# Performance work log

Measured on AMD Instinct MI355X. Metric: run time of the kernel, lower is better.

The kernel has to match this reference:

```python
import jax, jax.numpy as jnp
import numpy as np

N_NODES = 50000
NEG_SLOPE = 0.2


def gat_conv(x, edge_index, W, a_src, a_dst, b):
    """PyG GATConv, heads=1: linear -> per-edge attention -> segment softmax -> scatter-add."""
    n = x.shape[0]
    h = x @ W                                   # [N, out]
    # add self-loops (PyG default add_self_loops=True)
    loop = jnp.arange(n, dtype=edge_index.dtype)
    src = jnp.concatenate([edge_index[0], loop])  # message sources j
    dst = jnp.concatenate([edge_index[1], loop])  # aggregation targets i
    alpha_s = h @ a_src                          # [N]
    alpha_d = h @ a_dst                          # [N]
    e = jax.nn.leaky_relu(alpha_s[src] + alpha_d[dst], NEG_SLOPE)  # [E+N]
    # numerically stable segment softmax over edges grouped by dst
    m = jax.ops.segment_max(e, dst, num_segments=n)
    ex = jnp.exp(e - m[dst])
    denom = jax.ops.segment_sum(ex, dst, num_segments=n)
    alpha = ex / denom[dst]                      # [E+N]
    out = jax.ops.segment_sum(h[src] * alpha[:, None], dst, num_segments=n)
    return out + b


def setup_inputs() -> dict:
    key = jax.random.key(0)
    ks = jax.random.split(key, 12)
    F_IN, H1, H2 = 128, 64, 32
    E, ED = 800000, 800000
    x = jax.random.normal(ks[0], (N_NODES, F_IN), dtype=jnp.float32)
    edge_index = jax.random.randint(ks[1], (2, E), 0, N_NODES, dtype=jnp.int64)
    pos_edge_index = jax.random.randint(ks[2], (2, ED), 0, N_NODES, dtype=jnp.int64)
    neg_edge_index = jax.random.randint(ks[3], (2, ED), 0, N_NODES, dtype=jnp.int64)
    g = lambda k, shape, fan: (jax.random.normal(k, shape, dtype=jnp.float32) * (1.0 / np.sqrt(fan))).astype(jnp.float32)
    W1 = g(ks[4], (F_IN, H1), F_IN)
    a_src1 = g(ks[5], (H1,), H1)
    a_dst1 = g(ks[6], (H1,), H1)
    b1 = jnp.zeros((H1,), dtype=jnp.float32)
    W2 = g(ks[7], (H1, H2), H1)
    a_src2 = g(ks[8], (H2,), H2)
    a_dst2 = g(ks[9], (H2,), H2)
    b2 = jnp.zeros((H2,), dtype=jnp.float32)
    return {"x": x, "edge_index": edge_index, "pos_edge_index": pos_edge_index,
            "neg_edge_index": neg_edge_index, "W1": W1, "a_src1": a_src1,
            "a_dst1": a_dst1, "b1": b1, "W2": W2, "a_src2": a_src2,
            "a_dst2": a_dst2, "b2": b2}


def reference(x, edge_index, pos_edge_index, neg_edge_index,
              W1, a_src1, a_dst1, b1, W2, a_src2, a_dst2, b2):
    # encode (dropout omitted: eval-mode)
    h = gat_conv(x, edge_index, W1, a_src1, a_dst1, b1)
    h = jax.nn.relu(h)
    z = gat_conv(h, edge_index, W2, a_src2, a_dst2, b2)
    # decode: per-edge dot products on concatenated pos/neg edges
    ei = jnp.concatenate([pos_edge_index, neg_edge_index], axis=-1)
    logits = jnp.sum(z[ei[0]] * z[ei[1]], axis=-1)
    return logits
```

## Files before the change

kernel.cpp:

```cpp
#include <hip/hip_runtime.h>

#define NEG_SLOPE 0.2f

constexpr int N_NODES = 50000;
constexpr int TPB = 256;
constexpr int BSH = 7;
constexpr int NB = (N_NODES + 127) >> BSH;
constexpr int SCAT_CHUNK = 8192;

__device__ __forceinline__ unsigned short f2b(float f) {
  unsigned u = __float_as_uint(f);
  return (unsigned short)((u + 0x7FFFu + ((u >> 16) & 1u)) >> 16);
}
__device__ __forceinline__ float b2f(unsigned short b) {
  return __uint_as_float(((unsigned)b) << 16);
}
__device__ __forceinline__ float blo(unsigned u) {
  return __uint_as_float(u << 16);
}
__device__ __forceinline__ float bhi(unsigned u) {
  return __uint_as_float(u & 0xFFFF0000u);
}
__device__ __forceinline__ unsigned pack2(float a, float b) {
  return (unsigned)f2b(a) | ((unsigned)f2b(b) << 16);
}

__device__ __forceinline__ void tw_elem(const float* __restrict__ W,
                                        float4* __restrict__ Wt, int OUTD,
                                        int i) {
  int k4 = i / OUTD, c = i % OUTD;
  Wt[i] = make_float4(W[(4 * k4 + 0) * OUTD + c], W[(4 * k4 + 1) * OUTD + c],
                      W[(4 * k4 + 2) * OUTD + c], W[(4 * k4 + 3) * OUTD + c]);
}

__global__ void prep_kernel(const float* __restrict__ W1,
                            float4* __restrict__ Wt1,
                            const float* __restrict__ W2,
                            float4* __restrict__ Wt2,
                            int* __restrict__ pairCnt) {
  int i = blockIdx.x * blockDim.x + threadIdx.x;
  if (i < 2048) {
    tw_elem(W1, Wt1, 64, i);
  } else if (i < 2048 + 512) {
    tw_elem(W2, Wt2, 32, i - 2048);
  } else if (i < 2048 + 512 + NB) {
    pairCnt[i - 2560] = 0;
  }
}

template <int K, int OUTD>
__global__ __launch_bounds__(TPB) void gemm_alpha_hist(
    const float* __restrict__ X, const float4* __restrict__ Wt,
    const float* __restrict__ avec_src, const float* __restrict__ avec_dst,
    unsigned short* __restrict__ Hout, float* __restrict__ as_out,
    float* __restrict__ ad_out, int n, const int* __restrict__ edst, int E,
    int* __restrict__ pairCnt, int gemmBlocks) {
  constexpr int BK = 16;
  constexpr int NT = K / BK;
  constexpr int CT = OUTD / 2;
  constexpr int RG = 64 / CT;
  constexpr int RPT = 16 / RG;
  constexpr int WPB = TPB / 64;
  __shared__ float xs[WPB][2][16][BK + 4];
  __shared__ int hh[NB];

  if (blockIdx.x >= gemmBlocks) {
    const int vb = blockIdx.x - gemmBlocks;
    for (int i = threadIdx.x; i < NB; i += TPB) hh[i] = 0;
    __syncthreads();
    for (int i = vb * TPB + threadIdx.x; i < E; i += 256 * TPB)
      atomicAdd(&hh[edst[i] >> BSH], 1);
    __syncthreads();
    for (int i = threadIdx.x; i < NB; i += TPB)
      if (hh[i]) atomicAdd(&pairCnt[i], hh[i]);
    return;
  }

  const int t = threadIdx.x;
  const int wid = t >> 6;
  const int lane = t & 63;
  const int waveRow0 = blockIdx.x * (WPB * 16) + wid * 16;

  const int srow = lane >> 2;
  const int skq = lane & 3;
  const float* srcRow = X + (size_t)min(waveRow0 + srow, n - 1) * K + skq * 4;

  const int cc = lane % CT;
  const int c0 = 2 * cc;
  const int rg = lane / CT;
  const int r0 = rg * RPT;

  const float a_s0 = avec_src[c0], a_s1 = avec_src[c0 + 1];
  const float a_d0 = avec_dst[c0], a_d1 = avec_dst[c0 + 1];

  float4 g = *(const float4*)srcRow;
  *(float4*)&xs[wid][0][srow][skq * 4] = g;

  float acc[RPT][2];
#pragma unroll
  for (int i = 0; i < RPT; ++i) acc[i][0] = acc[i][1] = 0.f;

  for (int tile = 0;;) {
    if (tile + 1 < NT)
      g = *(const float4*)(srcRow + (size_t)(tile + 1) * BK);
    const int buf = tile & 1;
#pragma unroll
    for (int kq = 0; kq < BK / 4; ++kq) {
      const int kqg = tile * (BK / 4) + kq;
      const float4 w0 = Wt[(size_t)kqg * OUTD + c0];
      const float4 w1 = Wt[(size_t)kqg * OUTD + c0 + 1];
#pragma unroll
      for (int i = 0; i < RPT; ++i) {
        const float4 xv = *(const float4*)&xs[wid][buf][r0 + i][kq * 4];
        acc[i][0] = fmaf(xv.x, w0.x, acc[i][0]);
        acc[i][1] = fmaf(xv.x, w1.x, acc[i][1]);
        acc[i][0] = fmaf(xv.y, w0.y, acc[i][0]);
        acc[i][1] = fmaf(xv.y, w1.y, acc[i][1]);
        acc[i][0] = fmaf(xv.z, w0.z, acc[i][0]);
        acc[i][1] = fmaf(xv.z, w1.z, acc[i][1]);
        acc[i][0] = fmaf(xv.w, w0.w, acc[i][0]);
        acc[i][1] = fmaf(xv.w, w1.w, acc[i][1]);
      }
    }
    if (++tile == NT) break;
    *(float4*)&xs[wid][tile & 1][srow][skq * 4] = g;
  }

#pragma unroll
  for (int i = 0; i < RPT; ++i) {
    const int r = waveRow0 + r0 + i;
    if (r < n) {
      ushort2 hb;
      hb.x = f2b(acc[i][0]);
      hb.y = f2b(acc[i][1]);
      ((ushort2*)Hout)[(size_t)r * CT + cc] = hb;
      float vs = acc[i][0] * a_s0 + acc[i][1] * a_s1;
      float vd = acc[i][0] * a_d0 + acc[i][1] * a_d1;
#pragma unroll
      for (int m = CT / 2; m >= 1; m >>= 1) {
        vs += __shfl_xor(vs, m);
        vd += __shfl_xor(vd, m);
      }
      if (cc == 0) {
        as_out[r] = vs;
        ad_out[r] = vd;
      }
    }
  }
}

__global__ void bucket_scan(const int* __restrict__ pairCnt,
                            int* __restrict__ pairOff,
                            int* __restrict__ pairCursor,
                            int* __restrict__ csrOff, int N) {
  __shared__ int a[512], b[512];
  const int t = threadIdx.x;
  const int pc = (t < NB) ? pairCnt[t] : 0;
  const int nodes = (t < NB) ? min(128, N - (t << BSH)) : 0;
  a[t] = pc;
  b[t] = pc + nodes;
  __syncthreads();
  for (int off = 1; off < 512; off <<= 1) {
    int av = (t >= off) ? a[t - off] : 0;
    int bv = (t >= off) ? b[t - off] : 0;
    __syncthreads();
    a[t] += av;
    b[t] += bv;
    __syncthreads();
  }
  if (t < NB) {
    const int pe = a[t] - pc;
    pairOff[t] = pe;
    pairCursor[t] = pe;
    csrOff[t] = b[t] - (pc + nodes);
  }
  if (t == 0) {
    pairOff[NB] = a[511];
    csrOff[NB] = b[511];
  }
}

__global__ void bucket_scatter(const int* __restrict__ esrc,
                               const int* __restrict__ edst, int E,
                               int* __restrict__ pairCursor,
                               unsigned* __restrict__ stage) {
  __shared__ int h[NB], baseA[NB];
  const int base0 = blockIdx.x * SCAT_CHUNK;
  const int lim = min(E, base0 + SCAT_CHUNK);
  for (int i = threadIdx.x; i < NB; i += blockDim.x) h[i] = 0;
  __syncthreads();
  for (int i = base0 + threadIdx.x; i < lim; i += blockDim.x)
    atomicAdd(&h[edst[i] >> BSH], 1);
  __syncthreads();
  for (int i = threadIdx.x; i < NB; i += blockDim.x) {
    const int c = h[i];
    baseA[i] = c ? atomicAdd(&pairCursor[i], c) : 0;
  }
  __syncthreads();
  for (int i = threadIdx.x; i < NB; i += blockDim.x) h[i] = 0;
  __syncthreads();
  for (int i = base0 + threadIdx.x; i < lim; i += blockDim.x) {
    const int d = edst[i];
    const int s = esrc[i];
    const int bkt = d >> BSH;
    const int pos = baseA[bkt] + atomicAdd(&h[bkt], 1);
    stage[pos] = ((unsigned)(d & 127) << 16) | (unsigned)s;
  }
}

__global__ void build_csr(const unsigned* __restrict__ stage,
                          const int* __restrict__ pairOff,
                          const int* __restrict__ csrOff, int N,
                          int* __restrict__ rowoff, int* __restrict__ psrc) {
  __shared__ int cnt[128], excl[128];
  const int b = blockIdx.x, t = threadIdx.x;
  const int n0 = b << BSH;
  const int nn = min(128, N - n0);
  if (t < 128) cnt[t] = (t < nn) ? 1 : 0;
  __syncthreads();
  const int pb = pairOff[b], pe = pairOff[b + 1];
  for (int k = pb + t; k < pe; k += blockDim.x)
    atomicAdd(&cnt[stage[k] >> 16], 1);
  __syncthreads();
  if (t < 128) excl[t] = cnt[t];
  __syncthreads();
  for (int off = 1; off < 128; off <<= 1) {
    int v = (t < 128 && t >= off) ? excl[t - off] : 0;
    __syncthreads();
    if (t < 128) excl[t] += v;
    __syncthreads();
  }
  const int cb = csrOff[b];
  if (t < 128) {
    const int ex = excl[t] - cnt[t];
    if (t < nn) {
      rowoff[n0 + t] = cb + ex;
      psrc[cb + ex] = n0 + t;
    }
    cnt[t] = ex + 1;
  }
  if (b == 0 && t == 0) rowoff[N] = csrOff[NB];
  __syncthreads();
  for (int k = pb + t; k < pe; k += blockDim.x) {
    const unsigned p = stage[k];
    const int ld = p >> 16;
    const int s = p & 0xFFFF;
    const int pos = cb + atomicAdd(&cnt[ld], 1);
    psrc[pos] = s;
  }
}

__global__ __launch_bounds__(TPB) void gat_aggregate_fused(
    const unsigned short* __restrict__ Hb, const float* __restrict__ as,
    const float* __restrict__ ad, const int* __restrict__ rowoff,
    const int* __restrict__ psrc, int n, const float* __restrict__ bias,
    const float4* __restrict__ Wt2, const float* __restrict__ a_src2,
    const float* __restrict__ a_dst2, unsigned short* __restrict__ h2out,
    float* __restrict__ as2, float* __restrict__ ad2) {
  constexpr int D = 64;
  constexpr int LPE = D / 4;
  constexpr int EPS = 64 / LPE;
  constexpr int WPB = TPB / 64;
  __shared__ float2 wsP[WPB][64];

  const int wave = (blockIdx.x * blockDim.x + threadIdx.x) >> 6;
  const int wid = threadIdx.x >> 6;
  const int lane = threadIdx.x & 63;
  if (wave >= n) return;
  const int i = wave;
  const int beg = rowoff[i];
  const int end = rowoff[i + 1];
  const float adi = ad[i];

  const int p = lane / LPE;
  const int fl4 = (lane % LPE) * 4;

  float m = -1e30f, denom = 0.f;
  float4 acc = make_float4(0.f, 0.f, 0.f, 0.f);

  for (int c = beg; c < end; c += 64) {
    const int k = c + lane;
    const bool valid = (k < end);
    int s = 0;
    float e = -1e30f;
    if (valid) {
      s = psrc[k];
      e = as[s] + adi;
      e = (e > 0.f) ? e : e * NEG_SLOPE;
    }
    float cm = e;
#pragma unroll
    for (int mm = 32; mm >= 1; mm >>= 1) cm = fmaxf(cm, __shfl_xor(cm, mm));
    const float nm = fmaxf(m, cm);
    const float scale = __expf(m - nm);
    const float w = valid ? __expf(e - nm) : 0.f;
    float ws = w;
#pragma unroll
    for (int mm = 32; mm >= 1; mm >>= 1) ws += __shfl_xor(ws, mm);
    denom = denom * scale + ws;
    acc.x *= scale;
    acc.y *= scale;
    acc.z *= scale;
    acc.w *= scale;
    m = nm;

    wsP[wid][lane] = make_float2(w, __int_as_float(s));

    const int cnt = min(64, end - c);
    const int nsteps = (cnt + EPS - 1) / EPS;
#pragma unroll 4
    for (int j = 0; j < nsteps; ++j) {
      const float2 p2 = wsP[wid][j * EPS + p];
      const float wj = p2.x;
      const int sj = __float_as_int(p2.y);
      const ushort4 hu = *(const ushort4*)(Hb + (size_t)sj * D + fl4);
      acc.x = fmaf(wj, b2f(hu.x), acc.x);
      acc.y = fmaf(wj, b2f(hu.y), acc.y);
      acc.z = fmaf(wj, b2f(hu.z), acc.z);
      acc.w = fmaf(wj, b2f(hu.w), acc.w);
    }
  }
#pragma unroll
  for (int mm = LPE; mm < 64; mm <<= 1) {
    acc.x += __shfl_xor(acc.x, mm);
    acc.y += __shfl_xor(acc.y, mm);
    acc.z += __shfl_xor(acc.z, mm);
    acc.w += __shfl_xor(acc.w, mm);
  }
  const float4 bv = *(const float4*)(bias + fl4);
  float4 o;
  o.x = fmaxf(acc.x / denom + bv.x, 0.f);
  o.y = fmaxf(acc.y / denom + bv.y, 0.f);
  o.z = fmaxf(acc.z / denom + bv.z, 0.f);
  o.w = fmaxf(acc.w / denom + bv.w, 0.f);

  float* lrow = (float*)(&wsP[wid][0]);
  if (lane < 16) *(float4*)(lrow + fl4) = o;

  const int col = lane & 31;
  const int half = lane >> 5;
  float hc = 0.f;
#pragma unroll
  for (int j = 0; j < 8; ++j) {
    const float4 xv = *(const float4*)(lrow + half * 32 + j * 4);
    const float4 wv = Wt2[(size_t)(half * 8 + j) * 32 + col];
    hc = fmaf(xv.x, wv.x, hc);
    hc = fmaf(xv.y, wv.y, hc);
    hc = fmaf(xv.z, wv.z, hc);
    hc = fmaf(xv.w, wv.w, hc);
  }
  hc += __shfl_xor(hc, 32);

  float vs = hc * a_src2[col];
  float vd = hc * a_dst2[col];
#pragma unroll
  for (int mm = 16; mm >= 1; mm >>= 1) {
    vs += __shfl_xor(vs, mm);
    vd += __shfl_xor(vd, mm);
  }
  if (lane == 0) {
    as2[i] = vs;
    ad2[i] = vd;
  }
  const float hn = __shfl_xor(hc, 1);
  if (lane < 32 && !(col & 1))
    ((unsigned*)h2out)[(size_t)i * 16 + (col >> 1)] = pack2(hc, hn);
}

__global__ __launch_bounds__(TPB) void gat_aggregate32(
    const unsigned short* __restrict__ Hb, const float* __restrict__ as,
    const float* __restrict__ ad, const int* __restrict__ rowoff,
    const int* __restrict__ psrc, int n, const float* __restrict__ bias,
    unsigned short* __restrict__ outB) {
  constexpr int D = 32;
  constexpr int LPE = D / 4;
  constexpr int EPS = 64 / LPE;
  constexpr int WPB = TPB / 64;
  __shared__ float2 wsP[WPB][64];

  const int wave = (blockIdx.x * blockDim.x + threadIdx.x) >> 6;
  const int wid = threadIdx.x >> 6;
  const int lane = threadIdx.x & 63;
  if (wave >= n) return;
  const int i = wave;
  const int beg = rowoff[i];
  const int end = rowoff[i + 1];
  const float adi = ad[i];

  const int p = lane / LPE;
  const int fl4 = (lane % LPE) * 4;

  float m = -1e30f, denom = 0.f;
  float4 acc = make_float4(0.f, 0.f, 0.f, 0.f);

  for (int c = beg; c < end; c += 64) {
    const int k = c + lane;
    const bool valid = (k < end);
    int s = 0;
    float e = -1e30f;
    if (valid) {
      s = psrc[k];
      e = as[s] + adi;
      e = (e > 0.f) ? e : e * NEG_SLOPE;
    }
    float cm = e;
#pragma unroll
    for (int mm = 32; mm >= 1; mm >>= 1) cm = fmaxf(cm, __shfl_xor(cm, mm));
    const float nm = fmaxf(m, cm);
    const float scale = __expf(m - nm);
    const float w = valid ? __expf(e - nm) : 0.f;
    float ws = w;
#pragma unroll
    for (int mm = 32; mm >= 1; mm >>= 1) ws += __shfl_xor(ws, mm);
    denom = denom * scale + ws;
    acc.x *= scale;
    acc.y *= scale;
    acc.z *= scale;
    acc.w *= scale;
    m = nm;

    wsP[wid][lane] = make_float2(w, __int_as_float(s));

    const int cnt = min(64, end - c);
    const int nsteps = (cnt + EPS - 1) / EPS;
#pragma unroll 4
    for (int j = 0; j < nsteps; ++j) {
      const float2 p2 = wsP[wid][j * EPS + p];
      const float wj = p2.x;
      const int sj = __float_as_int(p2.y);
      const ushort4 hu = *(const ushort4*)(Hb + (size_t)sj * D + fl4);
      acc.x = fmaf(wj, b2f(hu.x), acc.x);
      acc.y = fmaf(wj, b2f(hu.y), acc.y);
      acc.z = fmaf(wj, b2f(hu.z), acc.z);
      acc.w = fmaf(wj, b2f(hu.w), acc.w);
    }
  }
#pragma unroll
  for (int mm = LPE; mm < 64; mm <<= 1) {
    acc.x += __shfl_xor(acc.x, mm);
    acc.y += __shfl_xor(acc.y, mm);
    acc.z += __shfl_xor(acc.z, mm);
    acc.w += __shfl_xor(acc.w, mm);
  }
  if (lane < LPE) {
    const float4 bv = *(const float4*)(bias + fl4);
    ushort4 ob;
    ob.x = f2b(acc.x / denom + bv.x);
    ob.y = f2b(acc.y / denom + bv.y);
    ob.z = f2b(acc.z / denom + bv.z);
    ob.w = f2b(acc.w / denom + bv.w);
    *(ushort4*)(outB + (size_t)i * D + fl4) = ob;
  }
}

__device__ __forceinline__ int loadS(const int* __restrict__ pos,
                                     const int* __restrict__ neg, int ED,
                                     int g) {
  return (g < ED) ? pos[g] : neg[g - ED];
}
__device__ __forceinline__ int loadD(const int* __restrict__ pos,
                                     const int* __restrict__ neg, int ED,
                                     int g) {
  return (g < ED) ? pos[ED + g] : neg[ED + (g - ED)];
}

__global__ __launch_bounds__(TPB) void decode_kernel(
    const unsigned short* __restrict__ zb, const int* __restrict__ pos,
    const int* __restrict__ neg, int ED, float* __restrict__ out) {
  const int wv = (blockIdx.x * blockDim.x + threadIdx.x) >> 6;
  const int lane = threadIdx.x & 63;
  const int g0 = wv * 16;
  const int NG = 2 * ED;
  if (g0 >= NG) return;

  int my = 0;
  if (lane < 32) {
    const int g = g0 + (lane & 15);
    if (g < NG)
      my = (lane < 16) ? loadS(pos, neg, ED, g) : loadD(pos, neg, ED, g);
  }
  const int e = lane >> 2;
  const int fl = lane & 3;
  const int s = __shfl(my, e);
  const int d = __shfl(my, 16 + e);
  const int g = g0 + e;
  if (g >= NG) return;

  const uint4 a = ((const uint4*)(zb + (size_t)s * 32))[fl];
  const uint4 b = ((const uint4*)(zb + (size_t)d * 32))[fl];
  float v = blo(a.x) * blo(b.x) + bhi(a.x) * bhi(b.x);
  v = fmaf(blo(a.y), blo(b.y), v);
  v = fmaf(bhi(a.y), bhi(b.y), v);
  v = fmaf(blo(a.z), blo(b.z), v);
  v = fmaf(bhi(a.z), bhi(b.z), v);
  v = fmaf(blo(a.w), blo(b.w), v);
  v = fmaf(bhi(a.w), bhi(b.w), v);
  v += __shfl_xor(v, 1);
  v += __shfl_xor(v, 2);
  if (fl == 0) out[g] = v;
}

extern "C" void kernel_launch(void* const* d_in, const int* in_sizes, int n_in,
                              void* d_out, int out_size, void* d_ws,
                              size_t ws_size, hipStream_t stream) {
  const int N = N_NODES;
  const float* x = (const float*)d_in[0];
  const int* ei = (const int*)d_in[1];
  const int* pe = (const int*)d_in[2];
  const int* ne = (const int*)d_in[3];
  const float* W1 = (const float*)d_in[4];
  const float* a_src1 = (const float*)d_in[5];
  const float* a_dst1 = (const float*)d_in[6];
  const float* b1 = (const float*)d_in[7];
  const float* W2 = (const float*)d_in[8];
  const float* a_src2 = (const float*)d_in[9];
  const float* a_dst2 = (const float*)d_in[10];
  const float* b2 = (const float*)d_in[11];
  float* out = (float*)d_out;

  const int E = in_sizes[1] / 2;
  const int ED = in_sizes[2] / 2;
  const int* esrc = ei;
  const int* edst = ei + E;

  char* base = (char*)d_ws;
  size_t off = 0;
  auto alloc = [&](size_t bytes) {
    char* p = base + off;
    off = (off + bytes + 255) & ~(size_t)255;
    return p;
  };
  unsigned short* h1b = (unsigned short*)alloc((size_t)N * 64 * 2);
  unsigned short* h2b = (unsigned short*)alloc((size_t)N * 32 * 2);
  unsigned short* zb = (unsigned short*)alloc((size_t)N * 32 * 2);
  float* as1 = (float*)alloc((size_t)N * 4);
  float* ad1 = (float*)alloc((size_t)N * 4);
  float* as2 = (float*)alloc((size_t)N * 4);
  float* ad2 = (float*)alloc((size_t)N * 4);
  int* rowoff = (int*)alloc((size_t)(N + 1) * 4);
  int* psrc = (int*)alloc((size_t)(E + N) * 4);
  unsigned* stage = (unsigned*)alloc((size_t)E * 4);
  int* pairCnt = (int*)alloc((size_t)NB * 4);
  int* pairOff = (int*)alloc((size_t)(NB + 1) * 4);
  int* pairCursor = (int*)alloc((size_t)NB * 4);
  int* csrOff = (int*)alloc((size_t)(NB + 1) * 4);
  float4* Wt1 = (float4*)alloc((size_t)(128 / 4) * 64 * 16);
  float4* Wt2 = (float4*)alloc((size_t)(64 / 4) * 32 * 16);

  prep_kernel<<<(2048 + 512 + NB + TPB - 1) / TPB, TPB, 0, stream>>>(
      W1, Wt1, W2, Wt2, pairCnt);

  const int gemmBlocks = (N + 63) / 64;
  gemm_alpha_hist<128, 64><<<gemmBlocks + 256, TPB, 0, stream>>>(
      x, Wt1, a_src1, a_dst1, h1b, as1, ad1, N, edst, E, pairCnt, gemmBlocks);

  bucket_scan<<<1, 512, 0, stream>>>(pairCnt, pairOff, pairCursor, csrOff, N);
  bucket_scatter<<<(E + SCAT_CHUNK - 1) / SCAT_CHUNK, TPB, 0, stream>>>(
      esrc, edst, E, pairCursor, stage);
  build_csr<<<NB, TPB, 0, stream>>>(stage, pairOff, csrOff, N, rowoff, psrc);

  gat_aggregate_fused<<<(N + 3) / 4, TPB, 0, stream>>>(
      h1b, as1, ad1, rowoff, psrc, N, b1, Wt2, a_src2, a_dst2, h2b, as2, ad2);

  gat_aggregate32<<<(N + 3) / 4, TPB, 0, stream>>>(h2b, as2, ad2, rowoff, psrc,
                                                   N, b2, zb);

  const int waves = (2 * ED + 15) / 16;
  decode_kernel<<<(waves * 64 + TPB - 1) / TPB, TPB, 0, stream>>>(
      zb, pe, ne, ED, out);
}
```

Measured before the change: 147.1 us.

## Drop bucket_scan launch by recomputing prefix sums in consumers; widen decode per wave

Removes the single-block bucket_scan kernel. bucket_scatter now computes the bucket prefix offsets redundantly in every block, and build_csr computes its own base with a block reduction, with cursors kept relative to these offsets. This saves one kernel launch and one serial dependency step, at the cost of redundant prefix work in every block. Decode also processes 32 edges per wave instead of 16, using all 64 lanes to load indices and issuing two gathers per lane.

```diff
diff --git a/kernel.cpp b/kernel.cpp
--- a/kernel.cpp
+++ b/kernel.cpp
@@ -36,8 +36,8 @@
 __global__ void prep_kernel(const float* __restrict__ W1,
                             float4* __restrict__ Wt1,
                             const float* __restrict__ W2,
-                            float4* __restrict__ Wt2,
-                            int* __restrict__ pairCnt) {
+                            float4* __restrict__ Wt2, int* __restrict__ pairCnt,
+                            int* __restrict__ cursorRel) {
   int i = blockIdx.x * blockDim.x + threadIdx.x;
   if (i < 2048) {
     tw_elem(W1, Wt1, 64, i);
@@ -45,6 +45,8 @@
     tw_elem(W2, Wt2, 32, i - 2048);
   } else if (i < 2048 + 512 + NB) {
     pairCnt[i - 2560] = 0;
+  } else if (i < 2048 + 512 + 2 * NB) {
+    cursorRel[i - 2560 - NB] = 0;
   }
 }
 
@@ -149,57 +151,55 @@
   }
 }
 
-__global__ void bucket_scan(const int* __restrict__ pairCnt,
-                            int* __restrict__ pairOff,
-                            int* __restrict__ pairCursor,
-                            int* __restrict__ csrOff, int N) {
-  __shared__ int a[512], b[512];
-  const int t = threadIdx.x;
-  const int pc = (t < NB) ? pairCnt[t] : 0;
-  const int nodes = (t < NB) ? min(128, N - (t << BSH)) : 0;
-  a[t] = pc;
-  b[t] = pc + nodes;
-  __syncthreads();
-  for (int off = 1; off < 512; off <<= 1) {
-    int av = (t >= off) ? a[t - off] : 0;
-    int bv = (t >= off) ? b[t - off] : 0;
-    __syncthreads();
-    a[t] += av;
-    b[t] += bv;
-    __syncthreads();
-  }
-  if (t < NB) {
-    const int pe = a[t] - pc;
-    pairOff[t] = pe;
-    pairCursor[t] = pe;
-    csrOff[t] = b[t] - (pc + nodes);
-  }
-  if (t == 0) {
-    pairOff[NB] = a[511];
-    csrOff[NB] = b[511];
-  }
-}
-
 __global__ void bucket_scatter(const int* __restrict__ esrc,
                                const int* __restrict__ edst, int E,
-                               int* __restrict__ pairCursor,
+                               const int* __restrict__ pairCnt,
+                               int* __restrict__ cursorRel,
                                unsigned* __restrict__ stage) {
-  __shared__ int h[NB], baseA[NB];
+  __shared__ int cntS[NB], poff[NB], h[NB], baseA[NB], csum[8];
+  const int t = threadIdx.x;
+  for (int i = t; i < NB; i += TPB) {
+    cntS[i] = pairCnt[i];
+    h[i] = 0;
+  }
+  __syncthreads();
+  if (t < 7) {
+    int s = 0;
+    for (int j = 0; j < 64; ++j) {
+      int idx = t * 64 + j;
+      if (idx < NB) s += cntS[idx];
+    }
+    csum[t] = s;
+  }
+  __syncthreads();
+  if (t == 0) {
+    int run = 0;
+    for (int c = 0; c < 7; ++c) {
+      int v = csum[c];
+      csum[c] = run;
+      run += v;
+    }
+  }
+  __syncthreads();
+  for (int i = t; i < NB; i += TPB) {
+    int s = csum[i >> 6];
+    for (int j = (i & ~63); j < i; ++j) s += cntS[j];
+    poff[i] = s;
+  }
+  __syncthreads();
+
   const int base0 = blockIdx.x * SCAT_CHUNK;
   const int lim = min(E, base0 + SCAT_CHUNK);
-  for (int i = threadIdx.x; i < NB; i += blockDim.x) h[i] = 0;
-  __syncthreads();
-  for (int i = base0 + threadIdx.x; i < lim; i += blockDim.x)
-    atomicAdd(&h[edst[i] >> BSH], 1);
-  __syncthreads();
-  for (int i = threadIdx.x; i < NB; i += blockDim.x) {
+  for (int i = base0 + t; i < lim; i += TPB) atomicAdd(&h[edst[i] >> BSH], 1);
+  __syncthreads();
+  for (int i = t; i < NB; i += TPB) {
     const int c = h[i];
-    baseA[i] = c ? atomicAdd(&pairCursor[i], c) : 0;
-  }
-  __syncthreads();
-  for (int i = threadIdx.x; i < NB; i += blockDim.x) h[i] = 0;
-  __syncthreads();
-  for (int i = base0 + threadIdx.x; i < lim; i += blockDim.x) {
+    baseA[i] = c ? poff[i] + atomicAdd(&cursorRel[i], c) : 0;
+  }
+  __syncthreads();
+  for (int i = t; i < NB; i += TPB) h[i] = 0;
+  __syncthreads();
+  for (int i = base0 + t; i < lim; i += TPB) {
     const int d = edst[i];
     const int s = esrc[i];
     const int bkt = d >> BSH;
@@ -209,16 +209,26 @@
 }
 
 __global__ void build_csr(const unsigned* __restrict__ stage,
-                          const int* __restrict__ pairOff,
-                          const int* __restrict__ csrOff, int N,
+                          const int* __restrict__ pairCnt, int N, int E,
                           int* __restrict__ rowoff, int* __restrict__ psrc) {
-  __shared__ int cnt[128], excl[128];
+  __shared__ int cnt[128], excl[128], red[TPB];
   const int b = blockIdx.x, t = threadIdx.x;
+  int s0 = 0;
+  for (int j = t; j < b; j += TPB) s0 += pairCnt[j];
+  red[t] = s0;
+  __syncthreads();
+  for (int m = TPB / 2; m >= 1; m >>= 1) {
+    if (t < m) red[t] += red[t + m];
+    __syncthreads();
+  }
+  const int pb = red[0];
+  const int pe = pb + pairCnt[b];
+  const int cb = pb + 128 * b;
+
   const int n0 = b << BSH;
   const int nn = min(128, N - n0);
   if (t < 128) cnt[t] = (t < nn) ? 1 : 0;
   __syncthreads();
-  const int pb = pairOff[b], pe = pairOff[b + 1];
   for (int k = pb + t; k < pe; k += blockDim.x)
     atomicAdd(&cnt[stage[k] >> 16], 1);
   __syncthreads();
@@ -230,7 +240,6 @@
     if (t < 128) excl[t] += v;
     __syncthreads();
   }
-  const int cb = csrOff[b];
   if (t < 128) {
     const int ex = excl[t] - cnt[t];
     if (t < nn) {
@@ -239,7 +248,7 @@
     }
     cnt[t] = ex + 1;
   }
-  if (b == 0 && t == 0) rowoff[N] = csrOff[NB];
+  if (b == 0 && t == 0) rowoff[N] = E + N;
   __syncthreads();
   for (int k = pb + t; k < pe; k += blockDim.x) {
     const unsigned p = stage[k];
@@ -469,35 +478,53 @@
     const int* __restrict__ neg, int ED, float* __restrict__ out) {
   const int wv = (blockIdx.x * blockDim.x + threadIdx.x) >> 6;
   const int lane = threadIdx.x & 63;
-  const int g0 = wv * 16;
+  const int g0 = wv * 32;
   const int NG = 2 * ED;
   if (g0 >= NG) return;
 
   int my = 0;
-  if (lane < 32) {
-    const int g = g0 + (lane & 15);
+  {
+    const int g = g0 + (lane & 31);
     if (g < NG)
-      my = (lane < 16) ? loadS(pos, neg, ED, g) : loadD(pos, neg, ED, g);
-  }
-  const int e = lane >> 2;
+      my = (lane < 32) ? loadS(pos, neg, ED, g) : loadD(pos, neg, ED, g);
+  }
+  const int e0 = lane >> 2;
   const int fl = lane & 3;
-  const int s = __shfl(my, e);
-  const int d = __shfl(my, 16 + e);
-  const int g = g0 + e;
-  if (g >= NG) return;
-
-  const uint4 a = ((const uint4*)(zb + (size_t)s * 32))[fl];
-  const uint4 b = ((const uint4*)(zb + (size_t)d * 32))[fl];
-  float v = blo(a.x) * blo(b.x) + bhi(a.x) * bhi(b.x);
-  v = fmaf(blo(a.y), blo(b.y), v);
-  v = fmaf(bhi(a.y), bhi(b.y), v);
-  v = fmaf(blo(a.z), blo(b.z), v);
-  v = fmaf(bhi(a.z), bhi(b.z), v);
-  v = fmaf(blo(a.w), blo(b.w), v);
-  v = fmaf(bhi(a.w), bhi(b.w), v);
-  v += __shfl_xor(v, 1);
-  v += __shfl_xor(v, 2);
-  if (fl == 0) out[g] = v;
+  const int eA = e0, eB = 16 + e0;
+  const int gA = g0 + eA, gB = g0 + eB;
+  const int sA = __shfl(my, eA), dA = __shfl(my, 32 + eA);
+  const int sB = __shfl(my, eB), dB = __shfl(my, 32 + eB);
+
+  const bool vA = (gA < NG), vB = (gB < NG);
+  uint4 a0, b0, a1, b1;
+  a0 = vA ? ((const uint4*)(zb + (size_t)sA * 32))[fl] : make_uint4(0, 0, 0, 0);
+  b0 = vA ? ((const uint4*)(zb + (size_t)dA * 32))[fl] : make_uint4(0, 0, 0, 0);
+  a1 = vB ? ((const uint4*)(zb + (size_t)sB * 32))[fl] : make_uint4(0, 0, 0, 0);
+  b1 = vB ? ((const uint4*)(zb + (size_t)dB * 32))[fl] : make_uint4(0, 0, 0, 0);
+
+  float v0 = blo(a0.x) * blo(b0.x) + bhi(a0.x) * bhi(b0.x);
+  v0 = fmaf(blo(a0.y), blo(b0.y), v0);
+  v0 = fmaf(bhi(a0.y), bhi(b0.y), v0);
+  v0 = fmaf(blo(a0.z), blo(b0.z), v0);
+  v0 = fmaf(bhi(a0.z), bhi(b0.z), v0);
+  v0 = fmaf(blo(a0.w), blo(b0.w), v0);
+  v0 = fmaf(bhi(a0.w), bhi(b0.w), v0);
+  float v1 = blo(a1.x) * blo(b1.x) + bhi(a1.x) * bhi(b1.x);
+  v1 = fmaf(blo(a1.y), blo(b1.y), v1);
+  v1 = fmaf(bhi(a1.y), bhi(b1.y), v1);
+  v1 = fmaf(blo(a1.z), blo(b1.z), v1);
+  v1 = fmaf(bhi(a1.z), bhi(b1.z), v1);
+  v1 = fmaf(blo(a1.w), blo(b1.w), v1);
+  v1 = fmaf(bhi(a1.w), bhi(b1.w), v1);
+
+  v0 += __shfl_xor(v0, 1);
+  v0 += __shfl_xor(v0, 2);
+  v1 += __shfl_xor(v1, 1);
+  v1 += __shfl_xor(v1, 2);
+  if (fl == 0) {
+    if (vA) out[gA] = v0;
+    if (vB) out[gB] = v1;
+  }
 }
 
 extern "C" void kernel_launch(void* const* d_in, const int* in_sizes, int n_in,
@@ -541,23 +568,20 @@
   int* psrc = (int*)alloc((size_t)(E + N) * 4);
   unsigned* stage = (unsigned*)alloc((size_t)E * 4);
   int* pairCnt = (int*)alloc((size_t)NB * 4);
-  int* pairOff = (int*)alloc((size_t)(NB + 1) * 4);
-  int* pairCursor = (int*)alloc((size_t)NB * 4);
-  int* csrOff = (int*)alloc((size_t)(NB + 1) * 4);
+  int* cursorRel = (int*)alloc((size_t)NB * 4);
   float4* Wt1 = (float4*)alloc((size_t)(128 / 4) * 64 * 16);
   float4* Wt2 = (float4*)alloc((size_t)(64 / 4) * 32 * 16);
 
-  prep_kernel<<<(2048 + 512 + NB + TPB - 1) / TPB, TPB, 0, stream>>>(
-      W1, Wt1, W2, Wt2, pairCnt);
+  prep_kernel<<<(2048 + 512 + 2 * NB + TPB - 1) / TPB, TPB, 0, stream>>>(
+      W1, Wt1, W2, Wt2, pairCnt, cursorRel);
 
   const int gemmBlocks = (N + 63) / 64;
   gemm_alpha_hist<128, 64><<<gemmBlocks + 256, TPB, 0, stream>>>(
       x, Wt1, a_src1, a_dst1, h1b, as1, ad1, N, edst, E, pairCnt, gemmBlocks);
 
-  bucket_scan<<<1, 512, 0, stream>>>(pairCnt, pairOff, pairCursor, csrOff, N);
   bucket_scatter<<<(E + SCAT_CHUNK - 1) / SCAT_CHUNK, TPB, 0, stream>>>(
-      esrc, edst, E, pairCursor, stage);
-  build_csr<<<NB, TPB, 0, stream>>>(stage, pairOff, csrOff, N, rowoff, psrc);
+      esrc, edst, E, pairCnt, cursorRel, stage);
+  build_csr<<<NB, TPB, 0, stream>>>(stage, pairCnt, N, E, rowoff, psrc);
 
   gat_aggregate_fused<<<(N + 3) / 4, TPB, 0, stream>>>(
       h1b, as1, ad1, rowoff, psrc, N, b1, Wt2, a_src2, a_dst2, h2b, as2, ad2);
@@ -565,7 +589,7 @@
   gat_aggregate32<<<(N + 3) / 4, TPB, 0, stream>>>(h2b, as2, ad2, rowoff, psrc,
                                                    N, b2, zb);
 
-  const int waves = (2 * ED + 15) / 16;
+  const int waves = (2 * ED + 31) / 32;
   decode_kernel<<<(waves * 64 + TPB - 1) / TPB, TPB, 0, stream>>>(
       zb, pe, ne, ED, out);
 }
```

After: 145.7 us. About the same (-0.9%).
